# Performance work log

Measured on AMD Instinct MI355X. Metric: run time of the kernel, lower is better.

Reference implementation:

```python
import jax, jax.numpy as jnp
import numpy as np

B, C, D_EMB = 512, 100000, 128
SCALE = 3.0
EPS = 1e-5


def _l2norm(x, eps=1e-12):
    # matches torch F.normalize(p=2, dim=-1)
    n = jnp.sqrt(jnp.sum(x * x, axis=-1, keepdims=True))
    return x / jnp.maximum(n, eps)


def setup_inputs() -> dict:
    key = jax.random.key(0)
    k1, k2, k3 = jax.random.split(key, 3)
    X = jax.random.normal(k1, (B, D_EMB), dtype=jnp.float32)
    indices = jnp.arange(B, dtype=jnp.int64)
    T = jax.random.randint(k2, (B,), 0, C).astype(jnp.int64)
    proxies = jax.random.normal(k3, (C, D_EMB), dtype=jnp.float32) / 8.0
    return {"X": X, "indices": indices, "T": T, "proxies": proxies}


def reference(X, indices, T, proxies):
    P = _l2norm(proxies)            # (C, D)
    Xn = _l2norm(X)                 # (B, D)

    # cross_attention -----------------------------------------------------
    Pb = P[T]                       # (B, D) gather of class proxies
    # affinity2boundary[b,k] = relu(<(Pb[b]+Pb[k])/2, Xn[k]>)
    #   = relu(0.5 * ((Pb @ Xn.T)[b,k] + diag[k]))  -- avoids (B,B,D) intermediate
    diag = jnp.sum(Pb * Xn, axis=-1)                       # (B,)
    aff2b = jax.nn.relu(0.5 * (Pb @ Xn.T + diag[None, :]))  # (B, B)
    aff2x = jax.nn.relu(Xn @ Xn.T)                          # (B, B)
    attention = aff2b + aff2x

    # NOTE: faithful to torch broadcasting: (B,B) / (B,) divides by COLUMN sums
    attention = attention / (attention.sum(-1) + EPS)       # (B, B)
    attention_weights = attention @ Xn                      # (B, D)
    X2 = Xn + attention_weights

    Ps = SCALE * _l2norm(P)         # (C, D), rows have norm SCALE
    Xs = SCALE * _l2norm(X2)        # (B, D)

    # squared pairwise distance block between X rows and proxy rows
    sx = jnp.sum(Xs * Xs, axis=-1)  # (B,)
    sp = jnp.sum(Ps * Ps, axis=-1)  # (C,)
    Dm = jnp.maximum(sx[:, None] + sp[None, :] - 2.0 * (Xs @ Ps.T), 0.0)  # (B, C)

    # one-hot targets (smoothing_const = 0) with masked log-softmax
    lsm = jax.nn.log_softmax(-Dm, axis=-1)                  # (B, C)
    loss = -lsm[jnp.arange(B), T]                           # (B,)
    return loss.mean()
```

## Files before the change

### kernel.cpp

```cpp
#include <hip/hip_runtime.h>
#include <hip/hip_bf16.h>
#include <math.h>

#define B_N 512
#define C_N 100000
#define CPAD 100032
#define D_N 128
#define NCHUNK (CPAD / 64)
#define K5_BLOCKS (CPAD / 4)
#define K6_GX 256
#define K6_GY 2
#define K6_BLOCKS (K6_GX * K6_GY)
#define PAD_CORR (32.0f * 1.522998e-8f)

typedef short short8 __attribute__((ext_vector_type(8)));
typedef float f32x4 __attribute__((ext_vector_type(4)));

__device__ __forceinline__ unsigned short f2bf(float f) {
  unsigned int u = __float_as_uint(f);
  u += 0x7fffu + ((u >> 16) & 1u);
  return (unsigned short)(u >> 16);
}

__device__ __forceinline__ void gl_lds16(const void* g, void* l) {
  __builtin_amdgcn_global_load_lds(
      (const __attribute__((address_space(1))) void*)g,
      (__attribute__((address_space(3))) void*)l, 16, 0, 0);
}

template <int NT>
__device__ __forceinline__ float block_reduce_sum(float v, float* red) {
  int t = threadIdx.x;
  __syncthreads();
  red[t] = v;
  __syncthreads();
#pragma unroll
  for (int s = NT / 2; s > 0; s >>= 1) {
    if (t < s) red[t] += red[t + s];
    __syncthreads();
  }
  return red[0];
}

__global__ __launch_bounds__(256) void kA(const float* __restrict__ X,
                                          const float* __restrict__ proxies,
                                          const int* __restrict__ T,
                                          float* __restrict__ Xn, float* __restrict__ Pb,
                                          float* __restrict__ diagv,
                                          unsigned short* __restrict__ Pnb,
                                          int* __restrict__ ctrs) {
  int bid = blockIdx.x;
  int t = threadIdx.x;
  if (bid < K5_BLOCKS) {
    int lane = t & 63;
    int row = bid * 4 + (t >> 6);
    float2 v = make_float2(0.f, 0.f);
    if (row < C_N) v = *(const float2*)(proxies + (size_t)row * D_N + 2 * lane);
    float ss = v.x * v.x + v.y * v.y;
#pragma unroll
    for (int off = 1; off < 64; off <<= 1) ss += __shfl_xor(ss, off);
    float inv = 1.f / fmaxf(sqrtf(ss), 1e-12f);
    unsigned short a = f2bf(v.x * inv), b = f2bf(v.y * inv);
    unsigned int pk = (unsigned int)a | ((unsigned int)b << 16);
    *(unsigned int*)(Pnb + (size_t)row * D_N + 2 * lane) = pk;
  } else {
    __shared__ float red[256];
    int b = bid - K5_BLOCKS;
    bool act = t < D_N;
    float v = act ? X[b * D_N + t] : 0.f;
    float ss = block_reduce_sum<256>(v * v, red);
    float xn = v / fmaxf(sqrtf(ss), 1e-12f);
    if (act) Xn[b * D_N + t] = xn;
    int row = T[b];
    float p = act ? proxies[(size_t)row * D_N + t] : 0.f;
    float ss2 = block_reduce_sum<256>(p * p, red);
    float pn = p / fmaxf(sqrtf(ss2), 1e-12f);
    if (act) Pb[b * D_N + t] = pn;
    float d = block_reduce_sum<256>(pn * xn, red);
    if (t == 0) {
      diagv[b] = d;
      if (b == 0) ctrs[32] = 0;
    }
  }
}

__global__ __launch_bounds__(512) void k3_att(const float* __restrict__ Xn,
                                              const float* __restrict__ Pb,
                                              const float* __restrict__ diagv,
                                              float* __restrict__ A, float* __restrict__ S) {
  __shared__ float xb[128], pbv[128];
  __shared__ float red[512];
  int b = blockIdx.x, t = threadIdx.x;
  if (t < 128) {
    xb[t] = Xn[b * D_N + t];
    pbv[t] = Pb[b * D_N + t];
  }
  __syncthreads();
  const float4* xr = (const float4*)(Xn + (size_t)t * D_N);
  float d1 = 0.f, d2 = 0.f;
#pragma unroll
  for (int i = 0; i < 32; i++) {
    float4 v = xr[i];
    d1 += pbv[4 * i] * v.x + pbv[4 * i + 1] * v.y + pbv[4 * i + 2] * v.z + pbv[4 * i + 3] * v.w;
    d2 += xb[4 * i] * v.x + xb[4 * i + 1] * v.y + xb[4 * i + 2] * v.z + xb[4 * i + 3] * v.w;
  }
  float a = fmaxf(0.5f * (d1 + diagv[t]), 0.f) + fmaxf(d2, 0.f);
  A[(size_t)b * B_N + t] = a;
  float rs = block_reduce_sum<512>(a, red);
  if (t == 0) S[b] = rs;
}

__global__ __launch_bounds__(512) void k4ab(const float* __restrict__ Xn,
                                            const float* __restrict__ Pb,
                                            const float* __restrict__ A,
                                            const float* __restrict__ S,
                                            unsigned short* __restrict__ Xsb,
                                            float* __restrict__ lossT,
                                            float* __restrict__ sumexpP) {
  __shared__ float xb[128], pbv[128];
  __shared__ float aw[512];
  __shared__ float red[512];
  int b = blockIdx.x, t = threadIdx.x;
  if (t < 128) {
    xb[t] = Xn[b * D_N + t];
    pbv[t] = Pb[b * D_N + t];
  }
  aw[t] = A[(size_t)b * B_N + t] / (S[t] + 1e-5f);
  __syncthreads();

  int d = t & 127, h = t >> 7;
  const float* xp = Xn + (size_t)(128 * h) * D_N + d;
  const float* awp = aw + 128 * h;
  float a0 = 0.f, a1 = 0.f, a2 = 0.f, a3 = 0.f;
#pragma unroll 8
  for (int kk = 0; kk < 128; kk += 4) {
    a0 = fmaf(awp[kk], xp[(size_t)kk * D_N], a0);
    a1 = fmaf(awp[kk + 1], xp[(size_t)(kk + 1) * D_N], a1);
    a2 = fmaf(awp[kk + 2], xp[(size_t)(kk + 2) * D_N], a2);
    a3 = fmaf(awp[kk + 3], xp[(size_t)(kk + 3) * D_N], a3);
  }
  red[t] = (a0 + a1) + (a2 + a3);
  __syncthreads();
  float x2 = (t < 128) ? (xb[t] + red[t] + red[t + 128] + red[t + 256] + red[t + 384]) : 0.f;

  float ss = block_reduce_sum<512>(x2 * x2, red);
  float xs = 3.f * x2 / fmaxf(sqrtf(ss), 1e-12f);
  if (t < 128) Xsb[b * D_N + t] = f2bf(xs);
  float dt = block_reduce_sum<512>((t < 128) ? xs * pbv[t] : 0.f, red);
  if (t == 0) {
    lossT[b] = fmaxf(18.f - 6.f * dt, 0.f);
    sumexpP[b * 16] = 0.f;
  }
}

__global__ __launch_bounds__(256, 2) void k6_big(const unsigned short* __restrict__ Pnb,
                                                 const unsigned short* __restrict__ Xsb,
                                                 float* __restrict__ sumexpP,
                                                 const float* __restrict__ lossT,
                                                 int* __restrict__ ctrs,
                                                 float* __restrict__ out) {
  __shared__ __align__(16) unsigned short sP[2][64 * 128];
  __shared__ float redf[256];
  __shared__ int sLast;
  const int t = threadIdx.x;
  const int w = t >> 6;
  const int lane = t & 63;
  const int lc = lane & 15;
  const int q = lane >> 4;
  const int b0 = blockIdx.y * 256;

  short8 afr[4][4];
#pragma unroll
  for (int mt = 0; mt < 4; mt++)
#pragma unroll
    for (int ks = 0; ks < 4; ks++)
      afr[mt][ks] = *(const short8*)(Xsb + (size_t)(b0 + 64 * w + 16 * mt + lc) * D_N +
                                     ks * 32 + q * 8);

  float pe[4][4];
#pragma unroll
  for (int mt = 0; mt < 4; mt++)
#pragma unroll
    for (int r = 0; r < 4; r++) pe[mt][r] = 0.f;

  const int rR = 16 * w + (lane >> 4);
  const int gsrc0 = (lane & 15);
#define STAGE(c0_, buf_)                                                              \
  {                                                                                   \
    _Pragma("unroll") for (int j = 0; j < 4; j++) {                                   \
      int R = rR + 4 * j;                                                             \
      int g = gsrc0 ^ ((R)&15);                                                       \
      gl_lds16(Pnb + (((size_t)(c0_) + R) << 7) + (g << 3),                           \
               &sP[buf_][w * 2048 + j * 512]);                                        \
    }                                                                                 \
  }

  int cc = blockIdx.x;
  STAGE(cc * 64, 0);
  int buf = 0;
  while (true) {
    int nc = cc + gridDim.x;
    if (nc < NCHUNK) STAGE(nc * 64, buf ^ 1);
    __builtin_amdgcn_sched_barrier(0);
    __builtin_amdgcn_s_waitcnt(0x0F74);
    __builtin_amdgcn_s_barrier();
    __builtin_amdgcn_sched_barrier(0);

    f32x4 acc[4][4];
#pragma unroll
    for (int mt = 0; mt < 4; mt++)
#pragma unroll
      for (int nt = 0; nt < 4; nt++) acc[mt][nt] = (f32x4){0.f, 0.f, 0.f, 0.f};

#pragma unroll
    for (int ks = 0; ks < 4; ks++) {
      short8 bfr[4];
#pragma unroll
      for (int nt = 0; nt < 4; nt++) {
        int R = 16 * nt + lc;
        int g = (ks * 4 + q) ^ lc;
        bfr[nt] = *(const short8*)(&sP[buf][R * 128 + (g << 3)]);
      }
#pragma unroll
      for (int nt = 0; nt < 4; nt++)
#pragma unroll
        for (int mt = 0; mt < 4; mt++)
          acc[mt][nt] = __builtin_amdgcn_mfma_f32_16x16x32_bf16(afr[mt][ks], bfr[nt],
                                                                acc[mt][nt], 0, 0, 0);
    }

#pragma unroll
    for (int mt = 0; mt < 4; mt++)
#pragma unroll
      for (int nt = 0; nt < 4; nt++) {
        f32x4 a = acc[mt][nt];
#pragma unroll
        for (int r = 0; r < 4; r++)
          pe[mt][r] += __builtin_amdgcn_exp2f(
              fminf(__fmaf_rn(8.65617024533378f, a[r], -25.9685107360013f), 0.f));
      }

    if (nc >= NCHUNK) break;
    __builtin_amdgcn_sched_barrier(0);
    __builtin_amdgcn_s_barrier();
    cc = nc;
    buf ^= 1;
  }

#pragma unroll
  for (int mt = 0; mt < 4; mt++) {
#pragma unroll
    for (int r = 0; r < 4; r++) {
      float p = pe[mt][r];
      p += __shfl_xor(p, 1);
      p += __shfl_xor(p, 2);
      p += __shfl_xor(p, 4);
      p += __shfl_xor(p, 8);
      if (lc == 0) {
        int rb = b0 + 64 * w + 16 * mt + 4 * q + r;
        atomicAdd(&sumexpP[rb * 16], p);
      }
    }
  }

  __builtin_amdgcn_s_waitcnt(0);
  if (t == 0) sLast = atomicAdd(&ctrs[32], 1);
  __syncthreads();
  if (sLast == K6_BLOCKS - 1) {
    float v = 0.f;
#pragma unroll
    for (int i = 0; i < 2; i++) {
      int b = t + 256 * i;
      float se = __hip_atomic_load(&sumexpP[b * 16], __ATOMIC_RELAXED,
                                   __HIP_MEMORY_SCOPE_AGENT);
      v += lossT[b] + logf(se - PAD_CORR);
    }
    float s = block_reduce_sum<256>(v, redf);
    if (t == 0) out[0] = s * (1.0f / 512.0f);
  }
}

extern "C" void kernel_launch(void* const* d_in, const int* in_sizes, int n_in,
                              void* d_out, int out_size, void* d_ws, size_t ws_size,
                              hipStream_t stream) {
  const float* X = (const float*)d_in[0];
  const int* T = (const int*)d_in[2];
  const float* proxies = (const float*)d_in[3];
  float* out = (float*)d_out;

  char* ws = (char*)d_ws;
  unsigned short* Pnb = (unsigned short*)ws;
  float* Xn = (float*)(ws + (size_t)CPAD * D_N * 2);
  float* Pb = Xn + B_N * D_N;
  float* X2 = Pb + B_N * D_N;
  float* dg = X2 + B_N * D_N;
  float* S = dg + B_N;
  float* lossT = S + B_N;
  float* sumexpP = lossT + B_N;
  unsigned short* Xsb = (unsigned short*)(sumexpP + B_N * 16);
  float* A = (float*)(Xsb + B_N * D_N);
  int* ctrs = (int*)(A + B_N * B_N);

  kA<<<K5_BLOCKS + B_N, 256, 0, stream>>>(X, proxies, T, Xn, Pb, dg, Pnb, ctrs);
  k3_att<<<B_N, 512, 0, stream>>>(Xn, Pb, dg, A, S);
  k4ab<<<B_N, 512, 0, stream>>>(Xn, Pb, A, S, Xsb, lossT, sumexpP);
  k6_big<<<dim3(K6_GX, K6_GY), 256, 0, stream>>>(Pnb, Xsb, sumexpP, lossT, ctrs, out);
}
```

Baseline: 152.9 us.

## Cover all 512 rows per k6 block and widen proxy normalization loads

The big distance/softmax kernel now uses 512-thread blocks that each hold all 512 X rows, instead of two grid rows of 256. Each proxy chunk is therefore staged into LDS once and reused by every row, which halves global reads of the bf16 proxy matrix. Wait counts are adjusted for the smaller per-thread staging. The proxy normalization pass now handles two rows per wave with float4 loads and 8-byte stores. The trade-offs are fewer total blocks and threads (grid of 256), possible register pressure at 512 threads with occupancy 2, and lower latency hiding.

```diff
diff --git a/kernel.cpp b/kernel.cpp
--- a/kernel.cpp
+++ b/kernel.cpp
@@ -7,10 +7,9 @@
 #define CPAD 100032
 #define D_N 128
 #define NCHUNK (CPAD / 64)
-#define K5_BLOCKS (CPAD / 4)
+#define KP_BLOCKS (CPAD / 8)
 #define K6_GX 256
-#define K6_GY 2
-#define K6_BLOCKS (K6_GX * K6_GY)
+#define K6_BLOCKS K6_GX
 #define PAD_CORR (32.0f * 1.522998e-8f)
 
 typedef short short8 __attribute__((ext_vector_type(8)));
@@ -51,21 +50,22 @@
                                           int* __restrict__ ctrs) {
   int bid = blockIdx.x;
   int t = threadIdx.x;
-  if (bid < K5_BLOCKS) {
-    int lane = t & 63;
-    int row = bid * 4 + (t >> 6);
-    float2 v = make_float2(0.f, 0.f);
-    if (row < C_N) v = *(const float2*)(proxies + (size_t)row * D_N + 2 * lane);
-    float ss = v.x * v.x + v.y * v.y;
-#pragma unroll
-    for (int off = 1; off < 64; off <<= 1) ss += __shfl_xor(ss, off);
+  if (bid < KP_BLOCKS) {
+    int w = t >> 6, lane = t & 63;
+    int half = lane >> 5, l32 = lane & 31;
+    int row = bid * 8 + w * 2 + half;
+    float4 v = make_float4(0.f, 0.f, 0.f, 0.f);
+    if (row < C_N) v = *(const float4*)(proxies + (size_t)row * D_N + 4 * l32);
+    float ss = v.x * v.x + v.y * v.y + v.z * v.z + v.w * v.w;
+#pragma unroll
+    for (int off = 1; off < 32; off <<= 1) ss += __shfl_xor(ss, off);
     float inv = 1.f / fmaxf(sqrtf(ss), 1e-12f);
-    unsigned short a = f2bf(v.x * inv), b = f2bf(v.y * inv);
-    unsigned int pk = (unsigned int)a | ((unsigned int)b << 16);
-    *(unsigned int*)(Pnb + (size_t)row * D_N + 2 * lane) = pk;
+    unsigned int p0 = (unsigned int)f2bf(v.x * inv) | ((unsigned int)f2bf(v.y * inv) << 16);
+    unsigned int p1 = (unsigned int)f2bf(v.z * inv) | ((unsigned int)f2bf(v.w * inv) << 16);
+    *(uint2*)(Pnb + (size_t)row * D_N + 4 * l32) = make_uint2(p0, p1);
   } else {
     __shared__ float red[256];
-    int b = bid - K5_BLOCKS;
+    int b = bid - KP_BLOCKS;
     bool act = t < D_N;
     float v = act ? X[b * D_N + t] : 0.f;
     float ss = block_reduce_sum<256>(v * v, red);
@@ -153,28 +153,27 @@
   }
 }
 
-__global__ __launch_bounds__(256, 2) void k6_big(const unsigned short* __restrict__ Pnb,
+__global__ __launch_bounds__(512, 2) void k6_big(const unsigned short* __restrict__ Pnb,
                                                  const unsigned short* __restrict__ Xsb,
                                                  float* __restrict__ sumexpP,
                                                  const float* __restrict__ lossT,
                                                  int* __restrict__ ctrs,
                                                  float* __restrict__ out) {
   __shared__ __align__(16) unsigned short sP[2][64 * 128];
-  __shared__ float redf[256];
+  __shared__ float redf[512];
   __shared__ int sLast;
   const int t = threadIdx.x;
   const int w = t >> 6;
   const int lane = t & 63;
   const int lc = lane & 15;
   const int q = lane >> 4;
-  const int b0 = blockIdx.y * 256;
 
   short8 afr[4][4];
 #pragma unroll
   for (int mt = 0; mt < 4; mt++)
 #pragma unroll
     for (int ks = 0; ks < 4; ks++)
-      afr[mt][ks] = *(const short8*)(Xsb + (size_t)(b0 + 64 * w + 16 * mt + lc) * D_N +
+      afr[mt][ks] = *(const short8*)(Xsb + (size_t)(64 * w + 16 * mt + lc) * D_N +
                                      ks * 32 + q * 8);
 
   float pe[4][4];
@@ -183,15 +182,15 @@
 #pragma unroll
     for (int r = 0; r < 4; r++) pe[mt][r] = 0.f;
 
-  const int rR = 16 * w + (lane >> 4);
+  const int rR = 8 * w + (lane >> 4);
   const int gsrc0 = (lane & 15);
 #define STAGE(c0_, buf_)                                                              \
   {                                                                                   \
-    _Pragma("unroll") for (int j = 0; j < 4; j++) {                                   \
+    _Pragma("unroll") for (int j = 0; j < 2; j++) {                                   \
       int R = rR + 4 * j;                                                             \
       int g = gsrc0 ^ ((R)&15);                                                       \
       gl_lds16(Pnb + (((size_t)(c0_) + R) << 7) + (g << 3),                           \
-               &sP[buf_][w * 2048 + j * 512]);                                        \
+               &sP[buf_][w * 1024 + j * 512]);                                        \
     }                                                                                 \
   }
 
@@ -200,9 +199,14 @@
   int buf = 0;
   while (true) {
     int nc = cc + gridDim.x;
-    if (nc < NCHUNK) STAGE(nc * 64, buf ^ 1);
-    __builtin_amdgcn_sched_barrier(0);
-    __builtin_amdgcn_s_waitcnt(0x0F74);
+    if (nc < NCHUNK) {
+      STAGE(nc * 64, buf ^ 1);
+      __builtin_amdgcn_sched_barrier(0);
+      __builtin_amdgcn_s_waitcnt(0x0F72);
+    } else {
+      __builtin_amdgcn_sched_barrier(0);
+      __builtin_amdgcn_s_waitcnt(0x0F70);
+    }
     __builtin_amdgcn_s_barrier();
     __builtin_amdgcn_sched_barrier(0);
 
@@ -257,7 +261,7 @@
       p += __shfl_xor(p, 4);
       p += __shfl_xor(p, 8);
       if (lc == 0) {
-        int rb = b0 + 64 * w + 16 * mt + 4 * q + r;
+        int rb = 64 * w + 16 * mt + 4 * q + r;
         atomicAdd(&sumexpP[rb * 16], p);
       }
     }
@@ -267,15 +271,10 @@
   if (t == 0) sLast = atomicAdd(&ctrs[32], 1);
   __syncthreads();
   if (sLast == K6_BLOCKS - 1) {
-    float v = 0.f;
-#pragma unroll
-    for (int i = 0; i < 2; i++) {
-      int b = t + 256 * i;
-      float se = __hip_atomic_load(&sumexpP[b * 16], __ATOMIC_RELAXED,
-                                   __HIP_MEMORY_SCOPE_AGENT);
-      v += lossT[b] + logf(se - PAD_CORR);
-    }
-    float s = block_reduce_sum<256>(v, redf);
+    float se = __hip_atomic_load(&sumexpP[t * 16], __ATOMIC_RELAXED,
+                                 __HIP_MEMORY_SCOPE_AGENT);
+    float v = lossT[t] + logf(se - PAD_CORR);
+    float s = block_reduce_sum<512>(v, redf);
     if (t == 0) out[0] = s * (1.0f / 512.0f);
   }
 }
@@ -301,8 +300,8 @@
   float* A = (float*)(Xsb + B_N * D_N);
   int* ctrs = (int*)(A + B_N * B_N);
 
-  kA<<<K5_BLOCKS + B_N, 256, 0, stream>>>(X, proxies, T, Xn, Pb, dg, Pnb, ctrs);
+  kA<<<KP_BLOCKS + B_N, 256, 0, stream>>>(X, proxies, T, Xn, Pb, dg, Pnb, ctrs);
   k3_att<<<B_N, 512, 0, stream>>>(Xn, Pb, dg, A, S);
   k4ab<<<B_N, 512, 0, stream>>>(Xn, Pb, A, S, Xsb, lossT, sumexpP);
-  k6_big<<<dim3(K6_GX, K6_GY), 256, 0, stream>>>(Pnb, Xsb, sumexpP, lossT, ctrs, out);
-}
+  k6_big<<<K6_GX, 512, 0, stream>>>(Pnb, Xsb, sumexpP, lossT, ctrs, out);
+}
```

Result: no change. 151.3 us (-1.1%).
